# Performance work log

Measured on AMD Instinct MI355X. Metric: run time of the kernel, lower is better.

Reference implementation:

```python
import jax, jax.numpy as jnp
import numpy as np
import math

MAX_ATOMS = 50
B = 2048
D = 512            # node_hidden_dim
MA = 512           # mol_a_repr_dim
ATT = 128          # attention dim
HID = 256          # mlp hidden width


def _counts():
    return (np.arange(B) % MAX_ATOMS) + 1  # deterministic ragged counts, sum = 52176


def _lin_params(key, din, dout):
    k1, k2 = jax.random.split(key)
    lim = 1.0 / math.sqrt(din)
    w = jax.random.uniform(k1, (din, dout), jnp.float32, -lim, lim)
    b = jax.random.uniform(k2, (dout,), jnp.float32, -lim, lim)
    return w, b


def mlp2(x, w1, b1, w2, b2):
    # create_mlp(in, out, [hidden]) => Linear -> ReLU -> Linear
    return jax.nn.relu(x @ w1 + b1) @ w2 + b2


def setup_inputs() -> dict:
    key = jax.random.key(0)
    ks = jax.random.split(key, 16)
    counts = _counts()
    N = int(counts.sum())  # 52176
    inp = {
        'mol_a_reprs': jax.random.normal(ks[0], (B, MA), jnp.float32),
        'node_hiddens': jax.random.normal(ks[1], (N, D), jnp.float32),
        'batch_counts': jnp.asarray(counts, jnp.int32),
    }
    wq1, bq1 = _lin_params(ks[2], D, HID); wq2, bq2 = _lin_params(ks[3], HID, ATT)
    wk1, bk1 = _lin_params(ks[4], D, HID); wk2, bk2 = _lin_params(ks[5], HID, ATT)
    wv1, bv1 = _lin_params(ks[6], D, HID); wv2, bv2 = _lin_params(ks[7], HID, ATT)
    uk1, ubk1 = _lin_params(ks[8], ATT, HID); uk2, ubk2 = _lin_params(ks[9], HID, ATT)
    uq1, ubq1 = _lin_params(ks[10], MA, HID); uq2, ubq2 = _lin_params(ks[11], HID, ATT)
    cs1, bcs1 = _lin_params(ks[12], MAX_ATOMS, 128); cs2, bcs2 = _lin_params(ks[13], 128, MAX_ATOMS)
    inp.update(dict(wq1=wq1, bq1=bq1, wq2=wq2, bq2=bq2,
                    wk1=wk1, bk1=bk1, wk2=wk2, bk2=bk2,
                    wv1=wv1, bv1=bv1, wv2=wv2, bv2=bv2,
                    uk1=uk1, ubk1=ubk1, uk2=uk2, ubk2=ubk2,
                    uq1=uq1, ubq1=ubq1, uq2=uq2, ubq2=ubq2,
                    cs1=cs1, bcs1=bcs1, cs2=cs2, bcs2=bcs2))
    return inp


def reference(mol_a_reprs, node_hiddens, batch_counts,
              wq1, bq1, wq2, bq2, wk1, bk1, wk2, bk2, wv1, bv1, wv2, bv2,
              uk1, ubk1, uk2, ubk2, uq1, ubq1, uq2, ubq2,
              cs1, bcs1, cs2, bcs2):
    N = node_hiddens.shape[0]
    offsets = jnp.concatenate([jnp.zeros((1,), jnp.int32),
                               jnp.cumsum(batch_counts)[:-1].astype(jnp.int32)])
    pos = jnp.arange(MAX_ATOMS, dtype=jnp.int32)                     # (M,)
    valid = pos[None, :] < batch_counts[:, None]                      # (B, M)
    gidx = jnp.clip(offsets[:, None] + pos[None, :], 0, N - 1)        # (B, M)
    # ragged gather -> padded (B, M, D), zeros at pad slots
    inp = jnp.where(valid[:, :, None], node_hiddens[gidx], 0.0)
    mask = ~valid                                                     # True where padded

    K = mlp2(inp, wk1, bk1, wk2, bk2)                                 # (B, M, 128)
    Q = mlp2(inp, wq1, bq1, wq2, bq2)
    V = mlp2(inp, wv1, bv1, wv2, bv2)
    KQT = jnp.einsum('bmd,bnd->bmn', K, Q)                            # (B, M, M)
    KQT = jnp.where(mask[:, :, None] | mask[:, None, :], -1e9, KQT)
    attn = jax.nn.softmax(KQT / math.sqrt(ATT), axis=-1)
    corr = jnp.einsum('bmn,bnd->bmd', attn, V)                        # (B, M, 128)

    K2 = mlp2(corr, uk1, ubk1, uk2, ubk2)                             # (B, M, 128)
    Q2 = mlp2(mol_a_reprs, uq1, ubq1, uq2, ubq2)                      # (B, 128)
    logits = jnp.einsum('bmd,bd->bm', K2, Q2) / math.sqrt(ATT)        # (B, M)
    sel = jax.nn.sigmoid(mlp2(logits, cs1, bcs1, cs2, bcs2))          # (B, M)

    # ragged scatter back to (N,); pad slots routed to dummy slot N
    sidx = jnp.where(valid, offsets[:, None] + pos[None, :], N)
    out = jnp.zeros((N + 1,), sel.dtype).at[sidx.reshape(-1)].set(sel.reshape(-1))
    return out[:N]
```

## Files before the change

kernel.cpp:

```cpp
#include <hip/hip_runtime.h>
#include <hip/hip_bf16.h>
#include <math.h>

#define DIM   512
#define HIDW  256
#define ATTW  128
#define MAXC  50
#define BLK   256
#define KW    128
#define HLW   128
#define HL2   264
#define BUFW  136
#define SB_W  52
#define CH    10
#define PXR   32
#define SCL   0.08838834764831845f

#define SWZ(row, e) ((e) ^ (((row) & 7) << 3))

#define AT_PA 12800
#define AT_KB 19200
#define AT_SM 32000

typedef float f32x4 __attribute__((ext_vector_type(4)));
typedef short s16x8 __attribute__((ext_vector_type(8)));

__device__ __forceinline__ float bf2f(ushort u){ union{unsigned i;float f;}v; v.i=((unsigned)u)<<16; return v.f; }
__device__ __forceinline__ ushort f2bf(float f){
  union{float f;unsigned i;}v; v.f=f;
  unsigned r = v.i + 0x7fffu + ((v.i>>16)&1u);
  return (ushort)(r>>16);
}
__device__ __forceinline__ s16x8 ldfrag(const ushort* p){ s16x8 v; __builtin_memcpy(&v, p, 16); return v; }
__device__ __forceinline__ f32x4 mfma16(s16x8 a, s16x8 b, f32x4 c){
  return __builtin_amdgcn_mfma_f32_16x16x32_bf16(a, b, c, 0, 0, 0);
}
__device__ __forceinline__ const ushort* fragp(const ushort* Wf, int ntile, int ktile, int KT, int L){
  return Wf + (((size_t)ntile*KT + ktile)*64 + L)*8;
}

template<bool F32>
__device__ __forceinline__ float ld(const void* p, int i){
  if (F32) return ((const float*)p)[i];
  return bf2f(((const ushort*)p)[i]);
}

struct P27 {
  const void *molA, *nodeH; const int* counts;
  const void *wq1,*bq1,*wq2,*bq2, *wk1,*bk1,*wk2,*bk2, *wv1,*bv1,*wv2,*bv2;
  const void *uk1,*ubk1,*uk2,*ubk2, *uq1,*ubq1,*uq2,*ubq2;
  const void *cs1,*bcs1,*cs2,*bcs2;
  void* out;
};

#define O_WK1T 0
#define O_WQ1T 131072
#define O_WV1T 262144
#define O_WK2T 393216
#define O_WQ2T 425984
#define O_WV2T 458752
#define O_UK1T 491520
#define O_UK2T 524288
#define WT_ELEMS   557056
#define O_UQ1TT 557056
#define O_UQ2TT 688128
#define WT2_ELEMS  720896
#define WT_T2ELEMS 393216
#define WT_BYTE_OFF 8704
#define Q2_BYTE_OFF (WT_BYTE_OFF + WT2_ELEMS*2)

__global__ void prep_kernel(const ushort* __restrict__ molAu,
                            const int* __restrict__ counts, int nb,
                            int* __restrict__ wsInt)
{
  __shared__ int part[BLK];
  __shared__ int cnt;
  const int t = threadIdx.x;
  if (t == 0) cnt = 0;
  __syncthreads();
  int e = (molAu[t] >> 7) & 0xFF;
  if (e >= 100 && e <= 140) atomicAdd(&cnt, 1);
  const int per = (nb + BLK - 1) / BLK;
  int s = 0;
  for (int i = 0; i < per; i++) { int idx = t*per + i; if (idx < nb) s += counts[idx]; }
  part[t] = s;
  __syncthreads();
  if (t == 0) {
    int run = 0;
    for (int i = 0; i < BLK; i++) { int v = part[i]; part[i] = run; run += v; }
    wsInt[0] = (cnt >= 220) ? 0 : 1;
  }
  __syncthreads();
  int run = part[t];
  for (int i = 0; i < per; i++) {
    int idx = t*per + i;
    if (idx < nb) { wsInt[4 + idx] = run; run += counts[idx]; }
  }
}

__global__ void transpose_wt(P27 P, const int* __restrict__ wsInt,
                             ushort* __restrict__ wt, unsigned long long cap_elems)
{
  unsigned i = blockIdx.x*BLK + threadIdx.x;
  if (i >= WT2_ELEMS) return;
  if ((unsigned long long)i >= cap_elems) return;
  const int f32m = wsInt[0];
  const void* src; unsigned j; int K, ldw;
  if (i < O_WK2T) {
    int m = i / 131072; j = i - m*131072;
    src = (m==0) ? P.wk1 : ((m==1) ? P.wq1 : P.wv1);
    K = 512; ldw = HIDW;
  } else if (i < O_UK1T) {
    int m = (i - O_WK2T) / 32768; j = (i - O_WK2T) - m*32768;
    src = (m==0) ? P.wk2 : ((m==1) ? P.wq2 : P.wv2);
    K = 256; ldw = ATTW;
  } else if (i < O_UK2T) {
    j = i - O_UK1T; src = P.uk1;  K = 128; ldw = HIDW;
  } else if (i < O_UQ1TT) {
    j = i - O_UK2T; src = P.uk2;  K = 256; ldw = ATTW;
  } else if (i < O_UQ2TT) {
    j = i - O_UQ1TT; src = P.uq1; K = 512; ldw = HIDW;
  } else {
    j = i - O_UQ2TT; src = P.uq2; K = 256; ldw = ATTW;
  }
  int tile = j >> 9, within = j & 511;
  int Lp = within >> 3, jj = within & 7;
  int l16 = Lp & 15, quad = Lp >> 4;
  int KT = K >> 5;
  int ntile = tile / KT, ktile = tile - ntile*KT;
  int n = ntile*16 + l16;
  int k = ktile*32 + quad*8 + jj;
  int idx = k*ldw + n;
  float v = f32m ? ((const float*)src)[idx] : bf2f(((const ushort*)src)[idx]);
  wt[i] = f2bf(v);
}

__global__ void __launch_bounds__(BLK, 3)
proj_kernel(P27 P, const int* __restrict__ wsInt, const ushort* __restrict__ wt,
            ushort* __restrict__ kqv, float* __restrict__ q2ws,
            long Nrows, int nb, int ntX)
{
  __shared__ __align__(16) ushort xs [PXR*DIM];
  __shared__ __align__(16) ushort hid[PXR*HIDW];
  const int t = threadIdx.x, bid = blockIdx.x;
  const int f32m = wsInt[0];
  const long NP = Nrows * ATTW;
  const bool isml = (bid >= ntX);
  const long r0 = isml ? (long)(bid - ntX)*PXR : (long)bid*PXR;
  int rows;
  const void* X;
  if (isml) { int rem = nb - (int)r0;        rows = (rem < PXR) ? rem : PXR; X = P.molA; }
  else      { long rem = Nrows - r0;         rows = (rem < PXR) ? (int)rem : PXR; X = P.nodeH; }
  if (rows <= 0) return;

  for (int i = t*8; i < PXR*DIM; i += BLK*8) {
    int row = i >> 9;
    int e   = i & (DIM-1);
    s16x8 o = {};
    if (row < rows) {
      if (f32m) {
        const float* xp = (const float*)X + (r0 + row)*DIM + e;
        f32x4 v0, v1; __builtin_memcpy(&v0, xp, 16); __builtin_memcpy(&v1, xp+4, 16);
#pragma unroll
        for (int q = 0; q < 4; q++) { o[q] = (short)f2bf(v0[q]); o[4+q] = (short)f2bf(v1[q]); }
      } else {
        o = ldfrag((const ushort*)X + (r0 + row)*DIM + e);
      }
    }
    __builtin_memcpy(&xs[row*DIM + SWZ(row, e)], &o, 16);
  }
  __syncthreads();

  const int w = t >> 6, L = t & 63, quad = L >> 4, l16 = L & 15;
  const int nsets = isml ? 1 : 3;
  for (int si = 0; si < nsets; si++) {
    const ushort *W1t, *W2t; const void *b1, *b2;
    if (isml)        { W1t = wt+O_UQ1TT; b1 = P.ubq1; W2t = wt+O_UQ2TT; b2 = P.ubq2; }
    else if (si==0)  { W1t = wt+O_WK1T;  b1 = P.bk1;  W2t = wt+O_WK2T;  b2 = P.bk2;  }
    else if (si==1)  { W1t = wt+O_WQ1T;  b1 = P.bq1;  W2t = wt+O_WQ2T;  b2 = P.bq2;  }
    else             { W1t = wt+O_WV1T;  b1 = P.bv1;  W2t = wt+O_WV2T;  b2 = P.bv2;  }

    f32x4 acc[2][4];
#pragma unroll
    for (int i = 0; i < 2; i++)
#pragma unroll
      for (int jn = 0; jn < 4; jn++) acc[i][jn] = (f32x4){0.f,0.f,0.f,0.f};
#pragma unroll 2
    for (int k0 = 0; k0 < DIM; k0 += 32) {
      const int kt = k0 >> 5;
      const int eo = SWZ(l16, k0 + quad*8);
      s16x8 a0 = ldfrag(xs + l16*DIM + eo);
      s16x8 a1 = ldfrag(xs + (16 + l16)*DIM + eo);
#pragma unroll
      for (int nt = 0; nt < 4; nt++) {
        s16x8 b = ldfrag(fragp(W1t, w*4 + nt, kt, 16, L));
        acc[0][nt] = mfma16(a0, b, acc[0][nt]);
        acc[1][nt] = mfma16(a1, b, acc[1][nt]);
      }
    }
    __syncthreads();
#pragma unroll
    for (int nt = 0; nt < 4; nt++) {
      int col = w*64 + nt*16 + l16;
      float bb = f32m ? ((const float*)b1)[col] : bf2f(((const ushort*)b1)[col]);
#pragma unroll
      for (int mt = 0; mt < 2; mt++)
#pragma unroll
        for (int r = 0; r < 4; r++) {
          int row = mt*16 + quad*4 + r;
          hid[row*HIDW + SWZ(row, col)] = f2bf(fmaxf(acc[mt][nt][r] + bb, 0.f));
        }
    }
    __syncthreads();

    f32x4 acc2[2][2];
#pragma unroll
    for (int i = 0; i < 2; i++) { acc2[i][0] = (f32x4){0.f,0.f,0.f,0.f}; acc2[i][1] = (f32x4){0.f,0.f,0.f,0.f}; }
#pragma unroll 2
    for (int k0 = 0; k0 < HIDW; k0 += 32) {
      const int kt = k0 >> 5;
      const int eo = SWZ(l16, k0 + quad*8);
      s16x8 a0 = ldfrag(hid + l16*HIDW + eo);
      s16x8 a1 = ldfrag(hid + (16 + l16)*HIDW + eo);
      s16x8 b0 = ldfrag(fragp(W2t, w*2,     kt, 8, L));
      s16x8 b1v= ldfrag(fragp(W2t, w*2 + 1, kt, 8, L));
      acc2[0][0] = mfma16(a0, b0,  acc2[0][0]);
      acc2[0][1] = mfma16(a0, b1v, acc2[0][1]);
      acc2[1][0] = mfma16(a1, b0,  acc2[1][0]);
      acc2[1][1] = mfma16(a1, b1v, acc2[1][1]);
    }
#pragma unroll
    for (int nt = 0; nt < 2; nt++) {
      int col = w*32 + nt*16 + l16;
      float bb = f32m ? ((const float*)b2)[col] : bf2f(((const ushort*)b2)[col]);
#pragma unroll
      for (int mt = 0; mt < 2; mt++)
#pragma unroll
        for (int r = 0; r < 4; r++) {
          int row = mt*16 + quad*4 + r;
          if (row < rows) {
            float v = acc2[mt][nt][r] + bb;
            if (isml) q2ws[(r0 + row)*ATTW + col] = v;
            else      kqv[(size_t)si*NP + (r0 + row)*ATTW + col] = f2bf(v);
          }
        }
    }
  }
}


__device__ __forceinline__ void scores_g(const ushort* __restrict__ Kp,
                                         const ushort* __restrict__ Qp,
                                         long offset, int c,
                                         float* __restrict__ sb, int t)
{
  const int w = t >> 6, L = t & 63, quad = L >> 4, l16 = L & 15;
  f32x4 acc[4];
#pragma unroll
  for (int i = 0; i < 4; i++) acc[i] = (f32x4){0.f,0.f,0.f,0.f};
  const int col = w*16 + l16;
  const long gq = offset + ((col < c) ? col : 0);
  long ga[4];
#pragma unroll
  for (int mt = 0; mt < 4; mt++) {
    int row = mt*16 + l16;
    ga[mt] = offset + ((row < c) ? row : 0);
  }
#pragma unroll
  for (int k0 = 0; k0 < ATTW; k0 += 32) {
    s16x8 b = ldfrag(Qp + (size_t)gq*ATTW + k0 + quad*8);
#pragma unroll
    for (int mt = 0; mt < 4; mt++) {
      s16x8 a = ldfrag(Kp + (size_t)ga[mt]*ATTW + k0 + quad*8);
      acc[mt] = mfma16(a, b, acc[mt]);
    }
  }
#pragma unroll
  for (int mt = 0; mt < 4; mt++)
#pragma unroll
    for (int r = 0; r < 4; r++) {
      int row = mt*16 + quad*4 + r;
      if (row < MAXC && col < MAXC)
        sb[row*SB_W + col] = (row < c && col < c) ? acc[mt][r]*SCL : -1e9f*SCL;
    }
}

__device__ __forceinline__ void softmax_pa(float* __restrict__ sb,
                                           ushort* __restrict__ pa, int c, int t)
{
  const int m = t >> 2, j = t & 3;
  if (m < MAXC) {
    float* row = sb + m*SB_W;
    float mx = -3.4e38f;
    for (int n = j; n < MAXC; n += 4) mx = fmaxf(mx, row[n]);
    mx = fmaxf(mx, __shfl_xor(mx, 1));
    mx = fmaxf(mx, __shfl_xor(mx, 2));
    float sum = 0.f;
    for (int n = j; n < MAXC; n += 4) { float e = expf(row[n] - mx); row[n] = e; sum += e; }
    sum += __shfl_xor(sum, 1);
    sum += __shfl_xor(sum, 2);
    float inv = 1.f / sum;
    for (int n = j; n < 64; n += 4)
      pa[m*64 + SWZ(m, n)] = (n < MAXC) ? f2bf(row[n] * inv) : (ushort)0;
  }
}

__device__ __forceinline__ void corr_half(const ushort* __restrict__ pa,
                                          const ushort* __restrict__ vt,
                                          ushort* __restrict__ dst, int colbase, int t)
{
  const int w = t >> 6, L = t & 63, quad = L >> 4, l16 = L & 15;
  f32x4 acc[4];
#pragma unroll
  for (int i = 0; i < 4; i++) acc[i] = (f32x4){0.f,0.f,0.f,0.f};
  const int dr = w*16 + l16;
#pragma unroll
  for (int k0 = 0; k0 < 64; k0 += 32) {
    s16x8 b = ldfrag(vt + dr*64 + SWZ(dr, k0 + quad*8));
#pragma unroll
    for (int mt = 0; mt < 4; mt++) {
      int row = mt*16 + l16;
      int ar = (row < MAXC) ? row : 0;
      s16x8 a = ldfrag(pa + ar*64 + SWZ(ar, k0 + quad*8));
      acc[mt] = mfma16(a, b, acc[mt]);
    }
  }
  const int col = colbase + w*16 + l16;
#pragma unroll
  for (int mt = 0; mt < 4; mt++)
#pragma unroll
    for (int r = 0; r < 4; r++) {
      int row = mt*16 + quad*4 + r;
      if (row < MAXC)
        dst[row*KW + SWZ(row, col)] = f2bf(acc[mt][r]);
    }
}

template<bool F32>
__device__ __forceinline__ void s1l_half(const ushort* __restrict__ src,
                                         const ushort* __restrict__ W1t,
                                         const void* __restrict__ Bv,
                                         ushort* __restrict__ hl, int t, int h)
{
  const int w = t >> 6, L = t & 63, quad = L >> 4, l16 = L & 15;
  f32x4 acc[4][2];
#pragma unroll
  for (int i = 0; i < 4; i++) { acc[i][0] = (f32x4){0.f,0.f,0.f,0.f}; acc[i][1] = (f32x4){0.f,0.f,0.f,0.f}; }
#pragma unroll
  for (int k0 = 0; k0 < ATTW; k0 += 32) {
    const int kt = k0 >> 5;
    s16x8 b0 = ldfrag(fragp(W1t, h*8 + w*2,     kt, 4, L));
    s16x8 b1 = ldfrag(fragp(W1t, h*8 + w*2 + 1, kt, 4, L));
#pragma unroll
    for (int mt = 0; mt < 4; mt++) {
      int row = mt*16 + l16;
      int ar = (row < MAXC) ? row : 0;
      s16x8 a = ldfrag(src + ar*KW + SWZ(ar, k0 + quad*8));
      acc[mt][0] = mfma16(a, b0, acc[mt][0]);
      acc[mt][1] = mfma16(a, b1, acc[mt][1]);
    }
  }
#pragma unroll
  for (int nt = 0; nt < 2; nt++) {
    int lcol = w*32 + nt*16 + l16;
    float bb = ld<F32>(Bv, h*128 + lcol);
#pragma unroll
    for (int mt = 0; mt < 4; mt++)
#pragma unroll
      for (int r = 0; r < 4; r++) {
        int row = mt*16 + quad*4 + r;
        if (row < MAXC)
          hl[row*HLW + SWZ(row, lcol)] = f2bf(fmaxf(acc[mt][nt][r] + bb, 0.f));
      }
  }
}

template<bool F32>
__device__ __forceinline__ void s2_partial(const ushort* __restrict__ hl,
                                           const ushort* __restrict__ W2t,
                                           int h, f32x4 (&acc)[4][2], int t)
{
  const int w = t >> 6, L = t & 63, quad = L >> 4, l16 = L & 15;
#pragma unroll
  for (int k0 = 0; k0 < 128; k0 += 32) {
    const int kt = h*4 + (k0 >> 5);
    s16x8 b0 = ldfrag(fragp(W2t, w*2,     kt, 8, L));
    s16x8 b1 = ldfrag(fragp(W2t, w*2 + 1, kt, 8, L));
#pragma unroll
    for (int mt = 0; mt < 4; mt++) {
      int row = mt*16 + l16;
      int ar = (row < MAXC) ? row : 0;
      s16x8 a = ldfrag(hl + ar*HLW + SWZ(ar, k0 + quad*8));
      acc[mt][0] = mfma16(a, b0, acc[mt][0]);
      acc[mt][1] = mfma16(a, b1, acc[mt][1]);
    }
  }
}

template<bool F32>
__device__ __forceinline__ void s2_store(f32x4 (&acc)[4][2], const void* __restrict__ Bv,
                                         ushort* __restrict__ dst, int t)
{
  const int w = t >> 6, L = t & 63, quad = L >> 4, l16 = L & 15;
#pragma unroll
  for (int nt = 0; nt < 2; nt++) {
    int col = w*32 + nt*16 + l16;
    float bb = ld<F32>(Bv, col);
#pragma unroll
    for (int mt = 0; mt < 4; mt++)
#pragma unroll
      for (int r = 0; r < 4; r++) {
        int row = mt*16 + quad*4 + r;
        if (row < MAXC)
          dst[row*KW + SWZ(row, col)] = f2bf(acc[mt][nt][r] + bb);
      }
  }
}

template<bool F32>
__device__ void attn_body(const P27& P, int b, int t, char* smem,
                          long offset, int c,
                          const ushort* __restrict__ wt,
                          const ushort* __restrict__ Kp, const ushort* __restrict__ Qp,
                          const ushort* __restrict__ Vp, const float* __restrict__ q2ws)
{
  float*  sb = (float*)smem;
  ushort* vt = (ushort*)smem;
  ushort* hl = (ushort*)smem;
  ushort* pa = (ushort*)(smem + AT_PA);
  ushort* kb = (ushort*)(smem + AT_KB);
  float* q2   = (float*)smem;
  float* lgt  = (float*)(smem + 512);
  float* selh = (float*)(smem + 768);

  scores_g(Kp, Qp, offset, c, sb, t);
  __syncthreads();
  softmax_pa(sb, pa, c, t);
  __syncthreads();

#pragma unroll
  for (int half = 0; half < 2; half++) {
    for (int i = t; i < 512; i += BLK) {
      int atom = i & 63, chunk = i >> 6;
      s16x8 f = {};
      if (atom < c) f = ldfrag(Vp + (size_t)(offset + atom)*ATTW + half*64 + chunk*8);
#pragma unroll
      for (int j = 0; j < 8; j++) {
        int d = chunk*8 + j;
        vt[d*64 + SWZ(d, atom)] = (ushort)f[j];
      }
    }
    __syncthreads();
    corr_half(pa, vt, kb, half*64, t);
    __syncthreads();
  }

  {
    f32x4 acc[4][2];
#pragma unroll
    for (int i = 0; i < 4; i++) { acc[i][0] = (f32x4){0.f,0.f,0.f,0.f}; acc[i][1] = (f32x4){0.f,0.f,0.f,0.f}; }
    s1l_half<F32>(kb, wt + O_UK1T, P.ubk1, hl, t, 0); __syncthreads();
    s2_partial<F32>(hl, wt + O_UK2T, 0, acc, t);      __syncthreads();
    s1l_half<F32>(kb, wt + O_UK1T, P.ubk1, hl, t, 1); __syncthreads();
    s2_partial<F32>(hl, wt + O_UK2T, 1, acc, t);
    s2_store<F32>(acc, P.ubk2, kb, t);
    __syncthreads();
  }

  if (t < ATTW) q2[t] = q2ws[(size_t)b*ATTW + t];
  __syncthreads();
  if (t < MAXC) {
    float s = 0.f;
    for (int k = 0; k < ATTW; k++)
      s += bf2f(kb[t*KW + SWZ(t, k)]) * q2[k];
    lgt[t] = s * SCL;
  }
  __syncthreads();
  if (t < ATTW) {
    float a = 0.f;
    for (int k = 0; k < MAXC; k++)
      a += lgt[k] * ld<F32>(P.cs1, k*ATTW + t);
    selh[t] = fmaxf(a + ld<F32>(P.bcs1, t), 0.f);
  }
  __syncthreads();
  if (t < c) {
    float a = 0.f;
    for (int k = 0; k < ATTW; k++)
      a += selh[k] * ld<F32>(P.cs2, k*MAXC + t);
    a += ld<F32>(P.bcs2, t);
    float v = 1.f / (1.f + expf(-a));
    if (F32) ((float*)P.out)[offset + t] = v;
    else     ((ushort*)P.out)[offset + t] = f2bf(v);
  }
}

__global__ void __launch_bounds__(BLK, 5)
attn_kernel(P27 P, const int* __restrict__ wsInt, const ushort* __restrict__ wt,
            const ushort* __restrict__ kqv, const float* __restrict__ q2ws, long Nrows)
{
  __shared__ __align__(16) char smem[AT_SM];
  const int t = threadIdx.x, b = blockIdx.x;
  const int f32m = wsInt[0];
  const long offset = wsInt[4 + b];
  const int c = P.counts[b];
  const long NP = Nrows * ATTW;
  const ushort* Kp = kqv;
  const ushort* Qp = kqv + NP;
  const ushort* Vp = kqv + 2*NP;
  if (f32m) attn_body<true >(P, b, t, smem, offset, c, wt, Kp, Qp, Vp, q2ws);
  else      attn_body<false>(P, b, t, smem, offset, c, wt, Kp, Qp, Vp, q2ws);
}

template<bool F32, bool XB>
__device__ __forceinline__ void stage1_mfma(const void* __restrict__ X, int xb, int c,
                                            const ushort* __restrict__ Wt,
                                            const void* __restrict__ Bv,
                                            ushort* __restrict__ hl, int hls, int t,
                                            int wlim)
{
  const int w = t >> 6, L = t & 63, quad = L >> 4, l16 = L & 15;
  f32x4 acc[4][4];
#pragma unroll
  for (int i = 0; i < 4; i++)
#pragma unroll
    for (int j = 0; j < 4; j++) acc[i][j] = (f32x4){0.f,0.f,0.f,0.f};

  bool va[4]; int rr[4];
#pragma unroll
  for (int mt = 0; mt < 4; mt++) {
    int row = mt*16 + l16;
    va[mt] = (row < c);
    rr[mt] = va[mt] ? row : 0;
  }

#pragma unroll 2
  for (int k0 = 0; k0 < DIM; k0 += 32) {
    const int kt = k0 >> 5;
    s16x8 a[4];
#pragma unroll
    for (int mt = 0; mt < 4; mt++) {
      s16x8 z = {};
      if (va[mt]) {
        if (XB || !F32) {
          a[mt] = ldfrag((const ushort*)X + xb + rr[mt]*DIM + k0 + quad*8);
        } else {
          const float* xp = (const float*)X + xb + rr[mt]*DIM + k0 + quad*8;
          f32x4 v0, v1;
          __builtin_memcpy(&v0, xp, 16);
          __builtin_memcpy(&v1, xp+4, 16);
          s16x8 v;
#pragma unroll
          for (int j = 0; j < 4; j++) { v[j] = (short)f2bf(v0[j]); v[4+j] = (short)f2bf(v1[j]); }
          a[mt] = v;
        }
      } else a[mt] = z;
    }
#pragma unroll
    for (int nt = 0; nt < 4; nt++) {
      s16x8 b = ldfrag(fragp(Wt, w*4 + nt, kt, 16, L));
#pragma unroll
      for (int mt = 0; mt < 4; mt++)
        acc[mt][nt] = mfma16(a[mt], b, acc[mt][nt]);
    }
  }
#pragma unroll
  for (int nt = 0; nt < 4; nt++) {
    int col = w*64 + nt*16 + l16;
    float bb = ld<F32>(Bv, col);
#pragma unroll
    for (int mt = 0; mt < 4; mt++)
#pragma unroll
      for (int r = 0; r < 4; r++) {
        int row = mt*16 + quad*4 + r;
        if (row < wlim)
          hl[row*hls + col] = f2bf(fmaxf(acc[mt][nt][r] + bb, 0.f));
      }
  }
}

template<bool F32>
__device__ void stage1_g(const void* X, int xb, int c,
                         const void* W, const void* Bv, ushort* hl, int t)
{
  for (int r0 = 0; r0 < MAXC; r0 += CH) {
    float acc[CH];
#pragma unroll
    for (int i = 0; i < CH; i++) acc[i] = 0.f;
    for (int k = 0; k < DIM; k++) {
      float wv = ld<F32>(W, k*HIDW + t);
#pragma unroll
      for (int i = 0; i < CH; i++) {
        int m = r0 + i;
        int mc = (m < c) ? m : 0;
        float xv = ld<F32>(X, xb + mc*DIM + k);
        acc[i] += ((m < c) ? xv : 0.f) * wv;
      }
    }
    float bb = ld<F32>(Bv, t);
#pragma unroll
    for (int i = 0; i < CH; i++)
      hl[(r0+i)*HIDW + t] = f2bf(fmaxf(acc[i] + bb, 0.f));
  }
}

template<bool F32>
__device__ void stage1_l(const ushort* S, const void* W, const void* Bv,
                         ushort* hl, int t)
{
  for (int r0 = 0; r0 < MAXC; r0 += CH) {
    float acc[CH];
#pragma unroll
    for (int i = 0; i < CH; i++) acc[i] = 0.f;
    for (int k = 0; k < ATTW; k++) {
      float wv = ld<F32>(W, k*HIDW + t);
#pragma unroll
      for (int i = 0; i < CH; i++)
        acc[i] += bf2f(S[(r0+i)*BUFW + k]) * wv;
    }
    float bb = ld<F32>(Bv, t);
#pragma unroll
    for (int i = 0; i < CH; i++)
      hl[(r0+i)*HIDW + t] = f2bf(fmaxf(acc[i] + bb, 0.f));
  }
}

template<bool F32>
__device__ void stage2(const void* W, const void* Bv, const ushort* hlp,
                       ushort* dst, int t)
{
  const int col = t & (ATTW-1);
  const int h = t >> 7;
  float bb = ld<F32>(Bv, col);
  for (int m = h; m < MAXC; m += 2) {
    float a = 0.f;
    for (int k = 0; k < HIDW; k++)
      a += bf2f(hlp[m*HIDW + k]) * ld<F32>(W, k*ATTW + col);
    dst[m*BUFW + col] = f2bf(a + bb);
  }
}

template<bool F32, bool MF>
__device__ void body(const P27& P, int b, int t,
                     ushort* hl, ushort* buf0, ushort* buf1, float* sb,
                     float* q2h, float* q2, float* logit, float* selh,
                     int offset, int c, const ushort* wt)
{
  const int xb = offset * DIM;

  if (MF) stage1_mfma<F32,false>(P.nodeH, xb, c, wt + O_WK1T, P.bk1, hl, HIDW, t, MAXC);
  else    stage1_g<F32>(P.nodeH, xb, c, P.wk1, P.bk1, hl, t);
  __syncthreads();
  stage2<F32>(P.wk2, P.bk2, hl, buf0, t);
  __syncthreads();
  if (MF) stage1_mfma<F32,false>(P.nodeH, xb, c, wt + O_WQ1T, P.bq1, hl, HIDW, t, MAXC);
  else    stage1_g<F32>(P.nodeH, xb, c, P.wq1, P.bq1, hl, t);
  __syncthreads();
  stage2<F32>(P.wq2, P.bq2, hl, buf1, t);
  __syncthreads();

  for (int idx = t; idx < MAXC*MAXC; idx += BLK) {
    int m = idx / MAXC, n = idx - m*MAXC;
    float s;
    if (m < c && n < c) {
      s = 0.f;
      for (int k = 0; k < ATTW; k++)
        s += bf2f(buf0[m*BUFW + k]) * bf2f(buf1[n*BUFW + k]);
    } else s = -1e9f;
    sb[m*SB_W + n] = s * SCL;
  }
  __syncthreads();
  if (t < MAXC) {
    float* row = sb + t*SB_W;
    float mx = row[0];
    for (int n = 1; n < MAXC; n++) mx = fmaxf(mx, row[n]);
    float sum = 0.f;
    for (int n = 0; n < MAXC; n++) { float e = expf(row[n] - mx); row[n] = e; sum += e; }
    float inv = 1.f / sum;
    for (int n = 0; n < MAXC; n++) row[n] *= inv;
  }
  __syncthreads();

  if (MF) stage1_mfma<F32,false>(P.nodeH, xb, c, wt + O_WV1T, P.bv1, hl, HIDW, t, MAXC);
  else    stage1_g<F32>(P.nodeH, xb, c, P.wv1, P.bv1, hl, t);
  __syncthreads();
  stage2<F32>(P.wv2, P.bv2, hl, buf0, t);
  __syncthreads();

  {
    const int col = t & (ATTW-1);
    const int h = t >> 7;
    for (int m = h; m < MAXC; m += 2) {
      float a = 0.f;
      for (int n = 0; n < MAXC; n++)
        a += sb[m*SB_W + n] * bf2f(buf0[n*BUFW + col]);
      buf1[m*BUFW + col] = f2bf(a);
    }
  }
  __syncthreads();

  stage1_l<F32>(buf1, P.uk1, P.ubk1, hl, t);
  __syncthreads();
  stage2<F32>(P.uk2, P.ubk2, hl, buf0, t);
  __syncthreads();

  {
    float a = 0.f;
    for (int k = 0; k < DIM; k++)
      a += ld<F32>(P.molA, b*DIM + k) * ld<F32>(P.uq1, k*HIDW + t);
    q2h[t] = fmaxf(a + ld<F32>(P.ubq1, t), 0.f);
  }
  __syncthreads();
  if (t < ATTW) {
    float a = 0.f;
    for (int k = 0; k < HIDW; k++)
      a += q2h[k] * ld<F32>(P.uq2, k*ATTW + t);
    q2[t] = a + ld<F32>(P.ubq2, t);
  }
  __syncthreads();
  if (t < MAXC) {
    float s = 0.f;
    for (int k = 0; k < ATTW; k++)
      s += bf2f(buf0[t*BUFW + k]) * q2[k];
    logit[t] = s * SCL;
  }
  __syncthreads();
  if (t < ATTW) {
    float a = 0.f;
    for (int k = 0; k < MAXC; k++)
      a += logit[k] * ld<F32>(P.cs1, k*ATTW + t);
    selh[t] = fmaxf(a + ld<F32>(P.bcs1, t), 0.f);
  }
  __syncthreads();
  if (t < c) {
    float a = 0.f;
    for (int k = 0; k < ATTW; k++)
      a += selh[k] * ld<F32>(P.cs2, k*MAXC + t);
    a += ld<F32>(P.bcs2, t);
    float v = 1.f / (1.f + expf(-a));
    if (F32) ((float*)P.out)[offset + t] = v;
    else     ((ushort*)P.out)[offset + t] = f2bf(v);
  }
}

__global__ void fused_mfma(P27 P, const int* __restrict__ wsInt, const ushort* __restrict__ wt)
{
  __shared__ __align__(16) ushort hl  [MAXC*HIDW];
  __shared__ __align__(16) ushort buf0[MAXC*BUFW];
  __shared__ __align__(16) ushort buf1[MAXC*BUFW];
  __shared__ __align__(16) float  sb  [MAXC*SB_W];
  __shared__ __align__(16) float  q2h [HIDW];
  __shared__ __align__(16) float  q2  [ATTW];
  __shared__ __align__(16) float  logit[64];
  __shared__ __align__(16) float  selh[ATTW];
  const int t = threadIdx.x, b = blockIdx.x;
  const int f32m = wsInt[0];
  const int offset = wsInt[4 + b];
  const int c = P.counts[b];
  if (f32m) body<true , true>(P, b, t, hl, buf0, buf1, sb, q2h, q2, logit, selh, offset, c, wt);
  else      body<false, true>(P, b, t, hl, buf0, buf1, sb, q2h, q2, logit, selh, offset, c, wt);
}

__global__ void fused_scalar(P27 P, const int* __restrict__ wsInt)
{
  __shared__ __align__(16) ushort hl  [MAXC*HIDW];
  __shared__ __align__(16) ushort buf0[MAXC*BUFW];
  __shared__ __align__(16) ushort buf1[MAXC*BUFW];
  __shared__ __align__(16) float  sb  [MAXC*SB_W];
  __shared__ __align__(16) float  q2h [HIDW];
  __shared__ __align__(16) float  q2  [ATTW];
  __shared__ __align__(16) float  logit[64];
  __shared__ __align__(16) float  selh[ATTW];
  const int t = threadIdx.x, b = blockIdx.x;
  const int f32m = wsInt[0];
  const int offset = wsInt[4 + b];
  const int c = P.counts[b];
  if (f32m) body<true , false>(P, b, t, hl, buf0, buf1, sb, q2h, q2, logit, selh, offset, c, nullptr);
  else      body<false, false>(P, b, t, hl, buf0, buf1, sb, q2h, q2, logit, selh, offset, c, nullptr);
}

extern "C" void kernel_launch(void* const* d_in, const int* in_sizes, int n_in,
                              void* d_out, int out_size, void* d_ws, size_t ws_size,
                              hipStream_t stream) {
  P27 P;
  P.molA  = d_in[0];
  P.nodeH = d_in[1];
  P.counts= (const int*)d_in[2];
  P.wq1 = d_in[3];  P.bq1 = d_in[4];  P.wq2 = d_in[5];  P.bq2 = d_in[6];
  P.wk1 = d_in[7];  P.bk1 = d_in[8];  P.wk2 = d_in[9];  P.bk2 = d_in[10];
  P.wv1 = d_in[11]; P.bv1 = d_in[12]; P.wv2 = d_in[13]; P.bv2 = d_in[14];
  P.uk1 = d_in[15]; P.ubk1= d_in[16]; P.uk2 = d_in[17]; P.ubk2= d_in[18];
  P.uq1 = d_in[19]; P.ubq1= d_in[20]; P.uq2 = d_in[21]; P.ubq2= d_in[22];
  P.cs1 = d_in[23]; P.bcs1= d_in[24]; P.cs2 = d_in[25]; P.bcs2= d_in[26];
  P.out = d_out;
  const int nb = in_sizes[2];
  int* wsInt = (int*)d_ws;

  prep_kernel<<<dim3(1), dim3(BLK), 0, stream>>>((const ushort*)d_in[0],
                                                 (const int*)d_in[2], nb, wsInt);

  const long xelems = (long)in_sizes[1];
  const long Nrows  = xelems / DIM;
  const int  ntX = (int)((Nrows + PXR - 1) / PXR);
  const int  ntA = (nb + PXR - 1) / PXR;

  size_t q2_off  = (size_t)Q2_BYTE_OFF;
  size_t kqv_off = (q2_off + (size_t)nb * ATTW * 4 + 255) & ~(size_t)255;
  const size_t need_new = kqv_off + (size_t)3 * Nrows * ATTW * 2;
  const size_t need2    = (size_t)WT_BYTE_OFF + (size_t)WT_T2ELEMS * 2;

  if (ws_size >= need_new) {
    ushort* wt   = (ushort*)((char*)d_ws + WT_BYTE_OFF);
    float*  q2ws = (float*)((char*)d_ws + q2_off);
    ushort* kqv  = (ushort*)((char*)d_ws + kqv_off);
    unsigned long long cap = (ws_size - WT_BYTE_OFF) / 2;
    transpose_wt<<<dim3((WT2_ELEMS + BLK - 1)/BLK), dim3(BLK), 0, stream>>>(P, wsInt, wt, cap);
    proj_kernel<<<dim3(ntX + ntA), dim3(BLK), 0, stream>>>(P, wsInt, wt, kqv, q2ws,
                                                           Nrows, nb, ntX);
    attn_kernel<<<dim3(nb), dim3(BLK), 0, stream>>>(P, wsInt, wt, kqv, q2ws, Nrows);
  } else if (ws_size >= need2) {
    ushort* wt = (ushort*)((char*)d_ws + WT_BYTE_OFF);
    unsigned long long cap = (ws_size - WT_BYTE_OFF) / 2;
    transpose_wt<<<dim3((WT2_ELEMS + BLK - 1)/BLK), dim3(BLK), 0, stream>>>(P, wsInt, wt, cap);
    fused_mfma<<<dim3(nb), dim3(BLK), 0, stream>>>(P, wsInt, wt);
  } else {
    fused_scalar<<<dim3(nb), dim3(BLK), 0, stream>>>(P, wsInt);
  }
}
```

Measured before the change: 412.5 us.

## Split projection kernel per weight set and load activations directly from global

The projection kernel now launches one block per (weight set, row tile) instead of looping over the K, Q and V sets inside a block. It drops the shared-memory staging of the input rows and loads A fragments straight from global memory, converting to bf16 in registers. The occupancy hint rises from 3 to 6 blocks per CU, helped by the smaller LDS footprint. The input rows are now read three times from global memory (once per set), trading extra L2/HBM traffic for more parallelism and higher occupancy.

Result: slower. 509.5 us (+23.5%).

```diff
diff --git a/kernel.cpp b/kernel.cpp
--- a/kernel.cpp
+++ b/kernel.cpp
@@ -135,117 +135,123 @@
   wt[i] = f2bf(v);
 }
 
-__global__ void __launch_bounds__(BLK, 3)
+template<bool F32>
+__device__ void proj_body_v3(const void* __restrict__ X, long r0, int rows,
+                             const ushort* __restrict__ W1t, const void* __restrict__ b1,
+                             const ushort* __restrict__ W2t, const void* __restrict__ b2,
+                             ushort* __restrict__ outb, float* __restrict__ outf,
+                             ushort* __restrict__ hid, int t)
+{
+  const int w = t >> 6, L = t & 63, quad = L >> 4, l16 = L & 15;
+  const long ra = r0 + ((l16      < rows) ? l16      : 0);
+  const long rb = r0 + ((16 + l16 < rows) ? 16 + l16 : 0);
+
+  f32x4 acc[2][4];
+#pragma unroll
+  for (int i = 0; i < 2; i++)
+#pragma unroll
+    for (int jn = 0; jn < 4; jn++) acc[i][jn] = (f32x4){0.f,0.f,0.f,0.f};
+#pragma unroll 2
+  for (int k0 = 0; k0 < DIM; k0 += 32) {
+    const int kt = k0 >> 5;
+    s16x8 a0, a1;
+    if (F32) {
+      const float* x0 = (const float*)X + ra*DIM + k0 + quad*8;
+      const float* x1 = (const float*)X + rb*DIM + k0 + quad*8;
+      f32x4 v0, v1, v2, v3;
+      __builtin_memcpy(&v0, x0, 16); __builtin_memcpy(&v1, x0+4, 16);
+      __builtin_memcpy(&v2, x1, 16); __builtin_memcpy(&v3, x1+4, 16);
+#pragma unroll
+      for (int q = 0; q < 4; q++) {
+        a0[q] = (short)f2bf(v0[q]); a0[4+q] = (short)f2bf(v1[q]);
+        a1[q] = (short)f2bf(v2[q]); a1[4+q] = (short)f2bf(v3[q]);
+      }
+    } else {
+      a0 = ldfrag((const ushort*)X + ra*DIM + k0 + quad*8);
+      a1 = ldfrag((const ushort*)X + rb*DIM + k0 + quad*8);
+    }
+#pragma unroll
+    for (int nt = 0; nt < 4; nt++) {
+      s16x8 b = ldfrag(fragp(W1t, w*4 + nt, kt, 16, L));
+      acc[0][nt] = mfma16(a0, b, acc[0][nt]);
+      acc[1][nt] = mfma16(a1, b, acc[1][nt]);
+    }
+  }
+#pragma unroll
+  for (int nt = 0; nt < 4; nt++) {
+    int col = w*64 + nt*16 + l16;
+    float bb = ld<F32>(b1, col);
+#pragma unroll
+    for (int mt = 0; mt < 2; mt++)
+#pragma unroll
+      for (int r = 0; r < 4; r++) {
+        int row = mt*16 + quad*4 + r;
+        hid[row*HIDW + SWZ(row, col)] = f2bf(fmaxf(acc[mt][nt][r] + bb, 0.f));
+      }
+  }
+  __syncthreads();
+
+  f32x4 acc2[2][2];
+#pragma unroll
+  for (int i = 0; i < 2; i++) { acc2[i][0] = (f32x4){0.f,0.f,0.f,0.f}; acc2[i][1] = (f32x4){0.f,0.f,0.f,0.f}; }
+#pragma unroll 2
+  for (int k0 = 0; k0 < HIDW; k0 += 32) {
+    const int kt = k0 >> 5;
+    const int eo = SWZ(l16, k0 + quad*8);
+    s16x8 a0 = ldfrag(hid + l16*HIDW + eo);
+    s16x8 a1 = ldfrag(hid + (16 + l16)*HIDW + eo);
+    s16x8 b0 = ldfrag(fragp(W2t, w*2,     kt, 8, L));
+    s16x8 b1v= ldfrag(fragp(W2t, w*2 + 1, kt, 8, L));
+    acc2[0][0] = mfma16(a0, b0,  acc2[0][0]);
+    acc2[0][1] = mfma16(a0, b1v, acc2[0][1]);
+    acc2[1][0] = mfma16(a1, b0,  acc2[1][0]);
+    acc2[1][1] = mfma16(a1, b1v, acc2[1][1]);
+  }
+#pragma unroll
+  for (int nt = 0; nt < 2; nt++) {
+    int col = w*32 + nt*16 + l16;
+    float bb = ld<F32>(b2, col);
+#pragma unroll
+    for (int mt = 0; mt < 2; mt++)
+#pragma unroll
+      for (int r = 0; r < 4; r++) {
+        int row = mt*16 + quad*4 + r;
+        if (row < rows) {
+          float v = acc2[mt][nt][r] + bb;
+          if (outb) outb[(r0 + row)*ATTW + col] = f2bf(v);
+          else      outf[(r0 + row)*ATTW + col] = v;
+        }
+      }
+  }
+}
+
+__global__ void __launch_bounds__(BLK, 6)
 proj_kernel(P27 P, const int* __restrict__ wsInt, const ushort* __restrict__ wt,
             ushort* __restrict__ kqv, float* __restrict__ q2ws,
             long Nrows, int nb, int ntX)
 {
-  __shared__ __align__(16) ushort xs [PXR*DIM];
   __shared__ __align__(16) ushort hid[PXR*HIDW];
   const int t = threadIdx.x, bid = blockIdx.x;
   const int f32m = wsInt[0];
   const long NP = Nrows * ATTW;
-  const bool isml = (bid >= ntX);
-  const long r0 = isml ? (long)(bid - ntX)*PXR : (long)bid*PXR;
-  int rows;
-  const void* X;
-  if (isml) { int rem = nb - (int)r0;        rows = (rem < PXR) ? rem : PXR; X = P.molA; }
-  else      { long rem = Nrows - r0;         rows = (rem < PXR) ? (int)rem : PXR; X = P.nodeH; }
+  int set, rt;
+  if (bid < 3*ntX) { set = bid / ntX; rt = bid - set*ntX; }
+  else             { set = 3;         rt = bid - 3*ntX; }
+  const long r0 = (long)rt * PXR;
+  int rows; const void* X;
+  if (set < 3) { long rem = Nrows - r0; rows = (rem < PXR) ? (int)rem : PXR; X = P.nodeH; }
+  else         { int rem = nb - (int)r0; rows = (rem < PXR) ? rem : PXR;     X = P.molA; }
   if (rows <= 0) return;
-
-  for (int i = t*8; i < PXR*DIM; i += BLK*8) {
-    int row = i >> 9;
-    int e   = i & (DIM-1);
-    s16x8 o = {};
-    if (row < rows) {
-      if (f32m) {
-        const float* xp = (const float*)X + (r0 + row)*DIM + e;
-        f32x4 v0, v1; __builtin_memcpy(&v0, xp, 16); __builtin_memcpy(&v1, xp+4, 16);
-#pragma unroll
-        for (int q = 0; q < 4; q++) { o[q] = (short)f2bf(v0[q]); o[4+q] = (short)f2bf(v1[q]); }
-      } else {
-        o = ldfrag((const ushort*)X + (r0 + row)*DIM + e);
-      }
-    }
-    __builtin_memcpy(&xs[row*DIM + SWZ(row, e)], &o, 16);
-  }
-  __syncthreads();
-
-  const int w = t >> 6, L = t & 63, quad = L >> 4, l16 = L & 15;
-  const int nsets = isml ? 1 : 3;
-  for (int si = 0; si < nsets; si++) {
-    const ushort *W1t, *W2t; const void *b1, *b2;
-    if (isml)        { W1t = wt+O_UQ1TT; b1 = P.ubq1; W2t = wt+O_UQ2TT; b2 = P.ubq2; }
-    else if (si==0)  { W1t = wt+O_WK1T;  b1 = P.bk1;  W2t = wt+O_WK2T;  b2 = P.bk2;  }
-    else if (si==1)  { W1t = wt+O_WQ1T;  b1 = P.bq1;  W2t = wt+O_WQ2T;  b2 = P.bq2;  }
-    else             { W1t = wt+O_WV1T;  b1 = P.bv1;  W2t = wt+O_WV2T;  b2 = P.bv2;  }
-
-    f32x4 acc[2][4];
-#pragma unroll
-    for (int i = 0; i < 2; i++)
-#pragma unroll
-      for (int jn = 0; jn < 4; jn++) acc[i][jn] = (f32x4){0.f,0.f,0.f,0.f};
-#pragma unroll 2
-    for (int k0 = 0; k0 < DIM; k0 += 32) {
-      const int kt = k0 >> 5;
-      const int eo = SWZ(l16, k0 + quad*8);
-      s16x8 a0 = ldfrag(xs + l16*DIM + eo);
-      s16x8 a1 = ldfrag(xs + (16 + l16)*DIM + eo);
-#pragma unroll
-      for (int nt = 0; nt < 4; nt++) {
-        s16x8 b = ldfrag(fragp(W1t, w*4 + nt, kt, 16, L));
-        acc[0][nt] = mfma16(a0, b, acc[0][nt]);
-        acc[1][nt] = mfma16(a1, b, acc[1][nt]);
-      }
-    }
-    __syncthreads();
-#pragma unroll
-    for (int nt = 0; nt < 4; nt++) {
-      int col = w*64 + nt*16 + l16;
-      float bb = f32m ? ((const float*)b1)[col] : bf2f(((const ushort*)b1)[col]);
-#pragma unroll
-      for (int mt = 0; mt < 2; mt++)
-#pragma unroll
-        for (int r = 0; r < 4; r++) {
-          int row = mt*16 + quad*4 + r;
-          hid[row*HIDW + SWZ(row, col)] = f2bf(fmaxf(acc[mt][nt][r] + bb, 0.f));
-        }
-    }
-    __syncthreads();
-
-    f32x4 acc2[2][2];
-#pragma unroll
-    for (int i = 0; i < 2; i++) { acc2[i][0] = (f32x4){0.f,0.f,0.f,0.f}; acc2[i][1] = (f32x4){0.f,0.f,0.f,0.f}; }
-#pragma unroll 2
-    for (int k0 = 0; k0 < HIDW; k0 += 32) {
-      const int kt = k0 >> 5;
-      const int eo = SWZ(l16, k0 + quad*8);
-      s16x8 a0 = ldfrag(hid + l16*HIDW + eo);
-      s16x8 a1 = ldfrag(hid + (16 + l16)*HIDW + eo);
-      s16x8 b0 = ldfrag(fragp(W2t, w*2,     kt, 8, L));
-      s16x8 b1v= ldfrag(fragp(W2t, w*2 + 1, kt, 8, L));
-      acc2[0][0] = mfma16(a0, b0,  acc2[0][0]);
-      acc2[0][1] = mfma16(a0, b1v, acc2[0][1]);
-      acc2[1][0] = mfma16(a1, b0,  acc2[1][0]);
-      acc2[1][1] = mfma16(a1, b1v, acc2[1][1]);
-    }
-#pragma unroll
-    for (int nt = 0; nt < 2; nt++) {
-      int col = w*32 + nt*16 + l16;
-      float bb = f32m ? ((const float*)b2)[col] : bf2f(((const ushort*)b2)[col]);
-#pragma unroll
-      for (int mt = 0; mt < 2; mt++)
-#pragma unroll
-        for (int r = 0; r < 4; r++) {
-          int row = mt*16 + quad*4 + r;
-          if (row < rows) {
-            float v = acc2[mt][nt][r] + bb;
-            if (isml) q2ws[(r0 + row)*ATTW + col] = v;
-            else      kqv[(size_t)si*NP + (r0 + row)*ATTW + col] = f2bf(v);
-          }
-        }
-    }
-  }
+  const ushort *W1t, *W2t; const void *b1, *b2;
+  ushort* ob = nullptr; float* of = nullptr;
+  switch (set) {
+    case 0: W1t = wt+O_WK1T;  b1 = P.bk1;  W2t = wt+O_WK2T;  b2 = P.bk2;  ob = kqv;        break;
+    case 1: W1t = wt+O_WQ1T;  b1 = P.bq1;  W2t = wt+O_WQ2T;  b2 = P.bq2;  ob = kqv + NP;   break;
+    case 2: W1t = wt+O_WV1T;  b1 = P.bv1;  W2t = wt+O_WV2T;  b2 = P.bv2;  ob = kqv + 2*NP; break;
+    default:W1t = wt+O_UQ1TT; b1 = P.ubq1; W2t = wt+O_UQ2TT; b2 = P.ubq2; of = q2ws;       break;
+  }
+  if (f32m) proj_body_v3<true >(X, r0, rows, W1t, b1, W2t, b2, ob, of, hid, t);
+  else      proj_body_v3<false>(X, r0, rows, W1t, b1, W2t, b2, ob, of, hid, t);
 }
 
 
@@ -814,8 +820,8 @@
     ushort* kqv  = (ushort*)((char*)d_ws + kqv_off);
     unsigned long long cap = (ws_size - WT_BYTE_OFF) / 2;
     transpose_wt<<<dim3((WT2_ELEMS + BLK - 1)/BLK), dim3(BLK), 0, stream>>>(P, wsInt, wt, cap);
-    proj_kernel<<<dim3(ntX + ntA), dim3(BLK), 0, stream>>>(P, wsInt, wt, kqv, q2ws,
-                                                           Nrows, nb, ntX);
+    proj_kernel<<<dim3(3*ntX + ntA), dim3(BLK), 0, stream>>>(P, wsInt, wt, kqv, q2ws,
+                                                             Nrows, nb, ntX);
     attn_kernel<<<dim3(nb), dim3(BLK), 0, stream>>>(P, wsInt, wt, kqv, q2ws, Nrows);
   } else if (ws_size >= need2) {
     ushort* wt = (ushort*)((char*)d_ws + WT_BYTE_OFF);
```
